# Kernel tuning notes

Hardware: AMD Instinct MI355X
Metric: run time of the kernel (lower is better)

Reference implementation:

```python
import jax, jax.numpy as jnp
import numpy as np

HEADS = 16
LN_EPS = 1e-5

def _ln(v, w, b):
    # LayerNorm over last dim (head dim s)
    mu = jnp.mean(v, axis=-1, keepdims=True)
    var = jnp.mean(jnp.square(v - mu), axis=-1, keepdims=True)
    return (v - mu) * jax.lax.rsqrt(var + LN_EPS) * w + b

def setup_inputs() -> dict:
    key = jax.random.key(0)
    ks = jax.random.split(key, 5)
    b, t, e = 2, 2048, 1024
    x = jax.random.normal(ks[0], (b, t, e), dtype=jnp.float32)
    scale = 0.02
    Wk = jax.random.normal(ks[1], (e, e), dtype=jnp.float32) * scale
    Wq = jax.random.normal(ks[2], (e, e), dtype=jnp.float32) * scale
    Wv = jax.random.normal(ks[3], (e, e), dtype=jnp.float32) * scale
    Wu = jax.random.normal(ks[4], (e, e), dtype=jnp.float32) * scale
    s = e // HEADS
    return {
        "x": x, "Wk": Wk, "Wq": Wq, "Wv": Wv, "Wu": Wu,
        "kln_w": jnp.ones((s,), jnp.float32), "kln_b": jnp.zeros((s,), jnp.float32),
        "qln_w": jnp.ones((s,), jnp.float32), "qln_b": jnp.zeros((s,), jnp.float32),
    }

def reference(x, Wk, Wq, Wv, Wu, kln_w, kln_b, qln_w, qln_b):
    b, t, e = x.shape
    h = HEADS
    s = e // h
    # nn.Linear: y = x @ W^T
    k = (x @ Wk.T).reshape(b, t, h, s)
    q = (x @ Wq.T).reshape(b, t, h, s)
    v = (x @ Wv.T).reshape(b, t, h, s)
    k = _ln(k, kln_w, kln_b)
    q = _ln(q, qln_w, qln_b)
    scalefactor = 1.0 / np.sqrt(s).astype(np.float32)
    # [b, h, t_q, t_k]
    dot = jnp.einsum('bqhs,bkhs->bhqk', q, k) * scalefactor
    causal = jnp.triu(jnp.ones((t, t), dtype=bool), k=1)  # mask strictly-upper (diag kept)
    dot = jnp.where(causal, -jnp.inf, dot)
    attn = jax.nn.softmax(dot, axis=-1)
    out = jnp.einsum('bhqk,bkhs->bqhs', attn, v).reshape(b, t, e)
    return out @ Wu.T
```

## Files before the change

kernel.cpp:

```cpp
#include <hip/hip_runtime.h>
#include <math.h>

#define T_SEQ 2048
#define E_DIM 1024
#define NH    16
#define HS    64
#define NB    2
#define M_ROWS 4096

typedef __attribute__((ext_vector_type(8))) short bf16x8;
typedef __attribute__((ext_vector_type(4))) short bf16x4;
typedef __attribute__((ext_vector_type(4))) float f32x4;

#define AS1 __attribute__((address_space(1)))
#define AS3 __attribute__((address_space(3)))

#define LOG2E 1.4426950408889634f

__device__ __forceinline__ f32x4 mfma16(bf16x4 a, bf16x4 b, f32x4 c) {
    return __builtin_amdgcn_mfma_f32_16x16x16bf16_1k(a, b, c, 0, 0, 0);
}

__device__ __forceinline__ ushort f2bf(float f) {
    union { float f; unsigned u; } c; c.f = f;
    unsigned r = c.u + 0x7fffu + ((c.u >> 16) & 1u);
    return (ushort)(r >> 16);
}
__device__ __forceinline__ ushort f2bf_trunc(float f) {
    union { float f; unsigned u; } c; c.f = f;
    return (ushort)(c.u >> 16);
}

__device__ __forceinline__ void load_lds16(const ushort* g, ushort* l) {
    __builtin_amdgcn_global_load_lds((const AS1 unsigned int*)g,
                                     (AS3 unsigned int*)l, 16, 0, 0);
}

__global__ __launch_bounds__(256) void cvt_all(
    const float* __restrict__ x,  const float* __restrict__ Wk,
    const float* __restrict__ Wq, const float* __restrict__ Wv,
    const float* __restrict__ Wu,
    ushort* __restrict__ xb,  ushort* __restrict__ Wkb,
    ushort* __restrict__ Wqb, ushort* __restrict__ Wvb,
    ushort* __restrict__ Wub)
{
    int i4 = blockIdx.x * 256 + threadIdx.x;
    int region = i4 >> 18;
    const float* src; ushort* dst; int off;
    if      (region < 4)  { src = x;  dst = xb;  off = i4; }
    else if (region == 4) { src = Wk; dst = Wkb; off = i4 - (4 << 18); }
    else if (region == 5) { src = Wq; dst = Wqb; off = i4 - (5 << 18); }
    else if (region == 6) { src = Wv; dst = Wvb; off = i4 - (6 << 18); }
    else                  { src = Wu; dst = Wub; off = i4 - (7 << 18); }
    float4 v = *(const float4*)(src + (size_t)off * 4);
    ushort4 o; o.x = f2bf(v.x); o.y = f2bf(v.y); o.z = f2bf(v.z); o.w = f2bf(v.w);
    *(ushort4*)(dst + (size_t)off * 4) = o;
}

__device__ __forceinline__ void gemm_core_db(
    const ushort* __restrict__ A, const ushort* __restrict__ W,
    int m0, int n0, ushort* As, ushort* Bs, f32x4 acc[4][4])
{
    const int tid  = threadIdx.x;
    const int lane = tid & 63, w = tid >> 6;
    const int quad = lane >> 4, l16 = lane & 15;
    const int wm = w & 1, wn = w >> 1;

    const int rl   = lane >> 2;
    const int gsw  = (lane & 3) ^ ((lane >> 3) & 3);
    const int fsw  = (l16 >> 1) & 3;

    const f32x4 zero = {0.f, 0.f, 0.f, 0.f};
#pragma unroll
    for (int mt = 0; mt < 4; ++mt)
#pragma unroll
        for (int nt = 0; nt < 4; ++nt) acc[mt][nt] = zero;

#pragma unroll
    for (int i = 0; i < 2; ++i) {
        int c = i * 4 + w;
        int row = c * 16 + rl;
        load_lds16(A + (size_t)(m0 + row) * E_DIM + gsw * 8, As + c * 512);
        load_lds16(W + (size_t)(n0 + row) * E_DIM + gsw * 8, Bs + c * 512);
    }

    for (int k0 = 0; k0 < E_DIM; k0 += 32) {
        const int buf = (k0 >> 5) & 1;
        ushort* Ab = As + buf * 4096;
        ushort* Bb = Bs + buf * 4096;
        __syncthreads();
        if (k0 + 32 < E_DIM) {
            ushort* An = As + (buf ^ 1) * 4096;
            ushort* Bn = Bs + (buf ^ 1) * 4096;
#pragma unroll
            for (int i = 0; i < 2; ++i) {
                int c = i * 4 + w;
                int row = c * 16 + rl;
                load_lds16(A + (size_t)(m0 + row) * E_DIM + k0 + 32 + gsw * 8,
                           An + c * 512);
                load_lds16(W + (size_t)(n0 + row) * E_DIM + k0 + 32 + gsw * 8,
                           Bn + c * 512);
            }
        }
        bf16x8 af[4], bfr[4];
#pragma unroll
        for (int mt = 0; mt < 4; ++mt)
            af[mt] = *(const bf16x8*)(Ab + (wm * 64 + mt * 16 + l16) * 32
                                      + ((quad ^ fsw) * 8));
#pragma unroll
        for (int nt = 0; nt < 4; ++nt)
            bfr[nt] = *(const bf16x8*)(Bb + (wn * 64 + nt * 16 + l16) * 32
                                       + ((quad ^ fsw) * 8));
#pragma unroll
        for (int mt = 0; mt < 4; ++mt)
#pragma unroll
            for (int nt = 0; nt < 4; ++nt)
                acc[mt][nt] = __builtin_amdgcn_mfma_f32_16x16x32_bf16(
                    af[mt], bfr[nt], acc[mt][nt], 0, 0, 0);
    }
}

__global__ __launch_bounds__(256) void gemm_qkv(
    const ushort* __restrict__ A,
    const ushort* __restrict__ W0, const ushort* __restrict__ W1,
    const ushort* __restrict__ W2,
    ushort* __restrict__ Kb, ushort* __restrict__ Qb, ushort* __restrict__ Vt,
    const float* __restrict__ kw, const float* __restrict__ kbias,
    const float* __restrict__ qw, const float* __restrict__ qbias)
{
    __shared__ ushort As[2 * 128 * 32];
    __shared__ ushort Bs[2 * 128 * 32];
    const int z = blockIdx.z;
    const ushort* W = (z == 0) ? W0 : (z == 1) ? W1 : W2;
    const int m0 = blockIdx.y * 128, n0 = blockIdx.x * 128;
    f32x4 acc[4][4];
    gemm_core_db(A, W, m0, n0, As, Bs, acc);

    const int lane = threadIdx.x & 63, w = threadIdx.x >> 6;
    const int quad = lane >> 4, l16 = lane & 15;
    const int wm = w & 1, wn = w >> 1;
    const int row0 = m0 + wm * 64;
    const int col0 = n0 + wn * 64;

    if (z < 2) {
        ushort* C = z ? Qb : Kb;
        const float* lw = z ? qw : kw;
        const float* lb = z ? qbias : kbias;
        const float scale = z ? (0.125f * LOG2E) : 1.0f;
        float wv[4], bv_[4];
#pragma unroll
        for (int nt = 0; nt < 4; ++nt) {
            wv[nt]  = lw[nt * 16 + l16];
            bv_[nt] = lb[nt * 16 + l16];
        }
#pragma unroll
        for (int mt = 0; mt < 4; ++mt)
#pragma unroll
            for (int r = 0; r < 4; ++r) {
                float v[4], d[4];
#pragma unroll
                for (int nt = 0; nt < 4; ++nt) v[nt] = acc[mt][nt][r];
                float s = v[0] + v[1] + v[2] + v[3];
                s += __shfl_xor(s, 1); s += __shfl_xor(s, 2);
                s += __shfl_xor(s, 4); s += __shfl_xor(s, 8);
                float mu = s * (1.0f / 64.0f);
                float q2 = 0.f;
#pragma unroll
                for (int nt = 0; nt < 4; ++nt) { d[nt] = v[nt] - mu; q2 += d[nt] * d[nt]; }
                q2 += __shfl_xor(q2, 1); q2 += __shfl_xor(q2, 2);
                q2 += __shfl_xor(q2, 4); q2 += __shfl_xor(q2, 8);
                float rin = rsqrtf(q2 * (1.0f / 64.0f) + 1e-5f);
                int row = row0 + mt * 16 + quad * 4 + r;
#pragma unroll
                for (int nt = 0; nt < 4; ++nt)
                    C[(size_t)row * E_DIM + col0 + nt * 16 + l16] =
                        f2bf((d[nt] * rin * wv[nt] + bv_[nt]) * scale);
            }
    } else {
        const int bidx = m0 >> 11;
        const int hh   = col0 >> 6;
        const int t0   = (m0 & 2047) + wm * 64;
#pragma unroll
        for (int mt = 0; mt < 4; ++mt)
#pragma unroll
            for (int nt = 0; nt < 4; ++nt) {
                ushort4 pk = make_ushort4(f2bf(acc[mt][nt][0]), f2bf(acc[mt][nt][1]),
                                          f2bf(acc[mt][nt][2]), f2bf(acc[mt][nt][3]));
                size_t off = ((size_t)(bidx * NH + hh) * 64 + nt * 16 + l16) * T_SEQ
                             + t0 + mt * 16 + quad * 4;
                *(ushort4*)(Vt + off) = pk;
            }
    }
}

__global__ __launch_bounds__(256) void gemm_o(
    const ushort* __restrict__ A, const ushort* __restrict__ W,
    float* __restrict__ C)
{
    __shared__ ushort As[2 * 128 * 32];
    __shared__ ushort Bs[2 * 128 * 32];
    const int m0 = blockIdx.y * 128, n0 = blockIdx.x * 128;
    f32x4 acc[4][4];
    gemm_core_db(A, W, m0, n0, As, Bs, acc);

    const int lane = threadIdx.x & 63, w = threadIdx.x >> 6;
    const int quad = lane >> 4, l16 = lane & 15;
    const int row0 = m0 + (w & 1) * 64;
    const int col0 = n0 + (w >> 1) * 64;
#pragma unroll
    for (int mt = 0; mt < 4; ++mt)
#pragma unroll
        for (int nt = 0; nt < 4; ++nt)
#pragma unroll
            for (int r = 0; r < 4; ++r)
                C[(size_t)(row0 + mt * 16 + quad * 4 + r) * E_DIM
                  + col0 + nt * 16 + l16] = acc[mt][nt][r];
}

__global__ __launch_bounds__(256, 4) void flash_attn5(
    const ushort* __restrict__ Qg, const ushort* __restrict__ Kg,
    const ushort* __restrict__ Vt, ushort* __restrict__ O)
{
    __shared__ ushort Ks[2][64 * 64];
    __shared__ ushort Vs[2][64 * 64];

    const int tid  = threadIdx.x;
    const int lane = tid & 63, w = tid >> 6;
    const int quad = lane >> 4, l16 = lane & 15;

    const int L = blockIdx.x;
    const int c = L & 255, s = L >> 8;
    const int q0 = c >> 5;
    const int bh = c & 31;
    const int qt = (s == 0) ? q0 : (s == 1) ? (15 - q0)
                 : (s == 2) ? (16 + q0) : (31 - q0);
    const int b = bh >> 4, h = bh & 15;

    const ushort* Qbase = Qg + ((size_t)b * T_SEQ) * E_DIM + h * HS;
    const ushort* Kbase = Kg + ((size_t)b * T_SEQ) * E_DIM + h * HS;
    const ushort* Vbase = Vt + ((size_t)bh * HS) * T_SEQ;

    const int rloc = lane >> 3;
    const int gswc = (lane & 7) ^ rloc;
    const int sw   = l16 & 7;

    bf16x8 aq[2];
#pragma unroll
    for (int ks = 0; ks < 2; ++ks)
        aq[ks] = *(const bf16x8*)(Qbase + (size_t)(qt * 64 + w * 16 + l16) * E_DIM
                                  + ks * 32 + quad * 8);

    const f32x4 zero = {0.f, 0.f, 0.f, 0.f};
    f32x4 o_acc[4];
#pragma unroll
    for (int dt = 0; dt < 4; ++dt) o_acc[dt] = zero;
    float l_acc = 0.f;

#pragma unroll
    for (int i = 0; i < 2; ++i) {
        int cc = w * 2 + i, row = cc * 8 + rloc;
        load_lds16(Kbase + (size_t)row * E_DIM + gswc * 8, Ks[0] + cc * 512);
        load_lds16(Vbase + (size_t)row * T_SEQ + gswc * 8, Vs[0] + cc * 512);
    }

    const float M8 = 8.0f * LOG2E;

    for (int jt = 0; jt <= qt; ++jt) {
        const int buf = jt & 1;
        __syncthreads();
        if (jt < qt) {
#pragma unroll
            for (int i = 0; i < 2; ++i) {
                int cc = w * 2 + i, row = cc * 8 + rloc;
                load_lds16(Kbase + (size_t)(jt + 1) * 64 * E_DIM
                           + (size_t)row * E_DIM + gswc * 8, Ks[buf ^ 1] + cc * 512);
                load_lds16(Vbase + (size_t)row * T_SEQ + (jt + 1) * 64 + gswc * 8,
                           Vs[buf ^ 1] + cc * 512);
            }
        }

        f32x4 sa[4];
#pragma unroll
        for (int nt = 0; nt < 4; ++nt) sa[nt] = zero;
#pragma unroll
        for (int ks = 0; ks < 2; ++ks) {
            int cp = ((ks * 4 + quad) ^ sw) * 8;
#pragma unroll
            for (int nt = 0; nt < 4; ++nt) {
                bf16x8 bk = *(const bf16x8*)(Ks[buf] + (nt * 16 + l16) * 64 + cp);
                sa[nt] = __builtin_amdgcn_mfma_f32_16x16x32_bf16(bk, aq[ks], sa[nt], 0, 0, 0);
            }
        }

        if (jt == qt) {
#pragma unroll
            for (int nt = 0; nt < 4; ++nt)
#pragma unroll
                for (int r = 0; r < 4; ++r)
                    if (nt * 16 + quad * 4 + r > w * 16 + l16) sa[nt][r] = -1e30f;
        }

        bf16x4 bp[4];
#pragma unroll
        for (int nt = 0; nt < 4; ++nt)
#pragma unroll
            for (int r = 0; r < 4; ++r) {
                float p = __builtin_amdgcn_exp2f(sa[nt][r] - M8);
                l_acc += p;
                bp[nt][r] = (short)f2bf_trunc(p);
            }

#pragma unroll
        for (int kt = 0; kt < 4; ++kt) {
            const int tt = kt * 16 + quad * 4;
            const int ch = tt >> 3, el = tt & 7;
#pragma unroll
            for (int dt = 0; dt < 4; ++dt) {
                const int vd = dt * 16 + l16;
                bf16x4 va = *(const bf16x4*)(Vs[buf] + vd * 64
                                             + ((ch ^ (vd & 7)) << 3) + el);
                o_acc[dt] = mfma16(va, bp[kt], o_acc[dt]);
            }
        }
    }

    l_acc += __shfl_xor(l_acc, 16);
    l_acc += __shfl_xor(l_acc, 32);
    const float inv = 1.0f / l_acc;
    const int trow = qt * 64 + w * 16 + l16;
#pragma unroll
    for (int dt = 0; dt < 4; ++dt) {
        ushort4 pk = make_ushort4(f2bf(o_acc[dt][0] * inv), f2bf(o_acc[dt][1] * inv),
                                  f2bf(o_acc[dt][2] * inv), f2bf(o_acc[dt][3] * inv));
        *(ushort4*)(O + ((size_t)b * T_SEQ + trow) * E_DIM + h * HS
                    + dt * 16 + quad * 4) = pk;
    }
}

extern "C" void kernel_launch(void* const* d_in, const int* in_sizes, int n_in,
                              void* d_out, int out_size, void* d_ws, size_t ws_size,
                              hipStream_t stream) {
    const float* x     = (const float*)d_in[0];
    const float* Wk    = (const float*)d_in[1];
    const float* Wq    = (const float*)d_in[2];
    const float* Wv    = (const float*)d_in[3];
    const float* Wu    = (const float*)d_in[4];
    const float* kln_w = (const float*)d_in[5];
    const float* kln_b = (const float*)d_in[6];
    const float* qln_w = (const float*)d_in[7];
    const float* qln_b = (const float*)d_in[8];
    float* out = (float*)d_out;

    const size_t NE = (size_t)M_ROWS * E_DIM;
    const size_t NW = (size_t)E_DIM * E_DIM;
    ushort* xb  = (ushort*)d_ws;
    ushort* Wkb = xb  + NE;
    ushort* Wqb = Wkb + NW;
    ushort* Wvb = Wqb + NW;
    ushort* Wub = Wvb + NW;
    ushort* Kb  = Wub + NW;
    ushort* Qb  = Kb  + NE;
    ushort* Vt  = Qb  + NE;
    ushort* Ob  = Vt  + NE;

    cvt_all<<<8192, 256, 0, stream>>>(x, Wk, Wq, Wv, Wu, xb, Wkb, Wqb, Wvb, Wub);

    gemm_qkv<<<dim3(E_DIM / 128, M_ROWS / 128, 3), 256, 0, stream>>>(
        xb, Wkb, Wqb, Wvb, Kb, Qb, Vt, kln_w, kln_b, qln_w, qln_b);

    flash_attn5<<<1024, 256, 0, stream>>>(Qb, Kb, Vt, Ob);

    gemm_o<<<dim3(E_DIM / 128, M_ROWS / 128), 256, 0, stream>>>(Ob, Wub, out);
}
```

Baseline: 182.0 us.

## Split causal attention KV range across two blocks with a separate merge kernel

Each (batch, head, query tile) is split into two blocks that each process half of the causal KV tiles. The blocks write unnormalized fp32 partial outputs and row sums to a workspace, and a new merge kernel adds the halves, normalizes and writes bf16. Blocks are ordered longest-first and use s_setprio around the MFMA sections, with the row-sum accumulation restructured as a tree. This is meant to balance load and raise parallelism, at the cost of an extra launch plus fp32 partial-result traffic. The shared fixed max offset keeps the merge a simple add.

```diff
diff --git a/kernel.cpp b/kernel.cpp
--- a/kernel.cpp
+++ b/kernel.cpp
@@ -217,9 +217,10 @@
                   + col0 + nt * 16 + l16] = acc[mt][nt][r];
 }
 
-__global__ __launch_bounds__(256, 4) void flash_attn5(
+__global__ __launch_bounds__(256, 4) void flash_attn6(
     const ushort* __restrict__ Qg, const ushort* __restrict__ Kg,
-    const ushort* __restrict__ Vt, ushort* __restrict__ O)
+    const ushort* __restrict__ Vt, float* __restrict__ Pbuf,
+    float* __restrict__ Lbuf)
 {
     __shared__ ushort Ks[2][64 * 64];
     __shared__ ushort Vs[2][64 * 64];
@@ -228,13 +229,19 @@
     const int lane = tid & 63, w = tid >> 6;
     const int quad = lane >> 4, l16 = lane & 15;
 
-    const int L = blockIdx.x;
-    const int c = L & 255, s = L >> 8;
-    const int q0 = c >> 5;
-    const int bh = c & 31;
-    const int qt = (s == 0) ? q0 : (s == 1) ? (15 - q0)
-                 : (s == 2) ? (16 + q0) : (31 - q0);
+    const int pair  = blockIdx.x >> 1;
+    const int split = blockIdx.x & 1;
+    const int bh = pair & 31;
+    const int qt = 31 - (pair >> 5);
     const int b = bh >> 4, h = bh & 15;
+
+    const int ntile = qt + 1;
+    const int hmid  = ntile >> 1;
+    const int jt0 = split ? hmid  : 0;
+    const int jt1 = split ? ntile : hmid;
+    if (jt0 >= jt1) return;
+
+    const int slot = (bh << 5) | qt;
 
     const ushort* Qbase = Qg + ((size_t)b * T_SEQ) * E_DIM + h * HS;
     const ushort* Kbase = Kg + ((size_t)b * T_SEQ) * E_DIM + h * HS;
@@ -259,16 +266,18 @@
 #pragma unroll
     for (int i = 0; i < 2; ++i) {
         int cc = w * 2 + i, row = cc * 8 + rloc;
-        load_lds16(Kbase + (size_t)row * E_DIM + gswc * 8, Ks[0] + cc * 512);
-        load_lds16(Vbase + (size_t)row * T_SEQ + gswc * 8, Vs[0] + cc * 512);
+        load_lds16(Kbase + (size_t)(jt0 * 64 + row) * E_DIM + gswc * 8,
+                   Ks[0] + cc * 512);
+        load_lds16(Vbase + (size_t)row * T_SEQ + jt0 * 64 + gswc * 8,
+                   Vs[0] + cc * 512);
     }
 
     const float M8 = 8.0f * LOG2E;
 
-    for (int jt = 0; jt <= qt; ++jt) {
-        const int buf = jt & 1;
+    for (int jt = jt0; jt < jt1; ++jt) {
+        const int buf = (jt - jt0) & 1;
         __syncthreads();
-        if (jt < qt) {
+        if (jt + 1 < jt1) {
 #pragma unroll
             for (int i = 0; i < 2; ++i) {
                 int cc = w * 2 + i, row = cc * 8 + rloc;
@@ -282,6 +291,7 @@
         f32x4 sa[4];
 #pragma unroll
         for (int nt = 0; nt < 4; ++nt) sa[nt] = zero;
+        __builtin_amdgcn_s_setprio(1);
 #pragma unroll
         for (int ks = 0; ks < 2; ++ks) {
             int cp = ((ks * 4 + quad) ^ sw) * 8;
@@ -291,6 +301,7 @@
                 sa[nt] = __builtin_amdgcn_mfma_f32_16x16x32_bf16(bk, aq[ks], sa[nt], 0, 0, 0);
             }
         }
+        __builtin_amdgcn_s_setprio(0);
 
         if (jt == qt) {
 #pragma unroll
@@ -301,15 +312,22 @@
         }
 
         bf16x4 bp[4];
-#pragma unroll
-        for (int nt = 0; nt < 4; ++nt)
-#pragma unroll
-            for (int r = 0; r < 4; ++r) {
-                float p = __builtin_amdgcn_exp2f(sa[nt][r] - M8);
-                l_acc += p;
-                bp[nt][r] = (short)f2bf_trunc(p);
-            }
-
+        float lp[4];
+#pragma unroll
+        for (int nt = 0; nt < 4; ++nt) {
+            float p0 = __builtin_amdgcn_exp2f(sa[nt][0] - M8);
+            float p1 = __builtin_amdgcn_exp2f(sa[nt][1] - M8);
+            float p2 = __builtin_amdgcn_exp2f(sa[nt][2] - M8);
+            float p3 = __builtin_amdgcn_exp2f(sa[nt][3] - M8);
+            bp[nt][0] = (short)f2bf_trunc(p0);
+            bp[nt][1] = (short)f2bf_trunc(p1);
+            bp[nt][2] = (short)f2bf_trunc(p2);
+            bp[nt][3] = (short)f2bf_trunc(p3);
+            lp[nt] = (p0 + p1) + (p2 + p3);
+        }
+        l_acc += (lp[0] + lp[1]) + (lp[2] + lp[3]);
+
+        __builtin_amdgcn_s_setprio(1);
 #pragma unroll
         for (int kt = 0; kt < 4; ++kt) {
             const int tt = kt * 16 + quad * 4;
@@ -322,18 +340,47 @@
                 o_acc[dt] = mfma16(va, bp[kt], o_acc[dt]);
             }
         }
+        __builtin_amdgcn_s_setprio(0);
     }
 
     l_acc += __shfl_xor(l_acc, 16);
     l_acc += __shfl_xor(l_acc, 32);
-    const float inv = 1.0f / l_acc;
-    const int trow = qt * 64 + w * 16 + l16;
-#pragma unroll
-    for (int dt = 0; dt < 4; ++dt) {
-        ushort4 pk = make_ushort4(f2bf(o_acc[dt][0] * inv), f2bf(o_acc[dt][1] * inv),
-                                  f2bf(o_acc[dt][2] * inv), f2bf(o_acc[dt][3] * inv));
-        *(ushort4*)(O + ((size_t)b * T_SEQ + trow) * E_DIM + h * HS
-                    + dt * 16 + quad * 4) = pk;
+    float* Po = Pbuf + (((size_t)split << 22) | ((size_t)slot << 12));
+    const int q = w * 16 + l16;
+#pragma unroll
+    for (int dt = 0; dt < 4; ++dt)
+        *(f32x4*)(Po + q * 64 + dt * 16 + quad * 4) = o_acc[dt];
+    if (quad == 0) Lbuf[(split << 16) | (slot << 6) | q] = l_acc;
+}
+
+__global__ __launch_bounds__(256) void attn_merge(
+    const float* __restrict__ Pbuf, const float* __restrict__ Lbuf,
+    ushort* __restrict__ O)
+{
+    const int slot = blockIdx.x;
+    const int bh = slot >> 5, qt = slot & 31;
+    const int b = bh >> 4, h = bh & 15;
+    const int tid = threadIdx.x;
+    const int dl = (tid & 15) * 4;
+    const int qh = tid >> 4;
+    const bool has0 = (qt > 0);
+    const float* P0 = Pbuf + ((size_t)slot << 12);
+    const float* P1 = P0 + ((size_t)1 << 22);
+#pragma unroll
+    for (int j = 0; j < 4; ++j) {
+        const int q = j * 16 + qh;
+        float l = Lbuf[(1 << 16) | (slot << 6) | q];
+        if (has0) l += Lbuf[(slot << 6) | q];
+        const float inv = 1.0f / l;
+        float4 c = *(const float4*)(P1 + q * 64 + dl);
+        if (has0) {
+            float4 a = *(const float4*)(P0 + q * 64 + dl);
+            c.x += a.x; c.y += a.y; c.z += a.z; c.w += a.w;
+        }
+        ushort4 pk = make_ushort4(f2bf(c.x * inv), f2bf(c.y * inv),
+                                  f2bf(c.z * inv), f2bf(c.w * inv));
+        *(ushort4*)(O + ((size_t)(b * T_SEQ + qt * 64 + q)) * E_DIM
+                    + h * HS + dl) = pk;
     }
 }
 
@@ -362,13 +409,16 @@
     ushort* Qb  = Kb  + NE;
     ushort* Vt  = Qb  + NE;
     ushort* Ob  = Vt  + NE;
+    float*  Pbuf = (float*)(Ob + NE);
+    float*  Lbuf = Pbuf + ((size_t)2 << 22);
 
     cvt_all<<<8192, 256, 0, stream>>>(x, Wk, Wq, Wv, Wu, xb, Wkb, Wqb, Wvb, Wub);
 
     gemm_qkv<<<dim3(E_DIM / 128, M_ROWS / 128, 3), 256, 0, stream>>>(
         xb, Wkb, Wqb, Wvb, Kb, Qb, Vt, kln_w, kln_b, qln_w, qln_b);
 
-    flash_attn5<<<1024, 256, 0, stream>>>(Qb, Kb, Vt, Ob);
+    flash_attn6<<<2048, 256, 0, stream>>>(Qb, Kb, Vt, Pbuf, Lbuf);
+    attn_merge<<<1024, 256, 0, stream>>>(Pbuf, Lbuf, Ob);
 
     gemm_o<<<dim3(E_DIM / 128, M_ROWS / 128), 256, 0, stream>>>(Ob, Wub, out);
 }
```

Measured after the change: 186.3 us. 1.02x slower.

## Rewrite QKV GEMM as 256x256-tile, 8-wave, 4-stage pipelined kernel

Applied to the files above, without the earlier changes.

Replaces the 128x128 double-buffered QKV GEMM with a 256x256-tile kernel using 512 threads, a 4-deep LDS ring fed by direct global-to-LDS loads, and explicit vmcnt waits and barriers. MFMA phases are interleaved with staging of A and B, with wave priority raised during compute. The three weight matrices are read as one contiguous concatenated Wqkv buffer, and a swizzled block index improves L2 locality. Larger tiles raise arithmetic intensity but need 128 KB of dynamic LDS, which limits occupancy, and the grid shrinks to 192 blocks on a GPU with more CUs than that.

```diff
diff --git a/kernel.cpp b/kernel.cpp
--- a/kernel.cpp
+++ b/kernel.cpp
@@ -120,27 +120,116 @@
     }
 }
 
-__global__ __launch_bounds__(256) void gemm_qkv(
-    const ushort* __restrict__ A,
-    const ushort* __restrict__ W0, const ushort* __restrict__ W1,
-    const ushort* __restrict__ W2,
+__global__ __launch_bounds__(512, 2) void gemm_qkv_8p(
+    const ushort* __restrict__ A, const ushort* __restrict__ Wqkv,
     ushort* __restrict__ Kb, ushort* __restrict__ Qb, ushort* __restrict__ Vt,
     const float* __restrict__ kw, const float* __restrict__ kbias,
     const float* __restrict__ qw, const float* __restrict__ qbias)
 {
-    __shared__ ushort As[2 * 128 * 32];
-    __shared__ ushort Bs[2 * 128 * 32];
-    const int z = blockIdx.z;
-    const ushort* W = (z == 0) ? W0 : (z == 1) ? W1 : W2;
-    const int m0 = blockIdx.y * 128, n0 = blockIdx.x * 128;
-    f32x4 acc[4][4];
-    gemm_core_db(A, W, m0, n0, As, Bs, acc);
-
-    const int lane = threadIdx.x & 63, w = threadIdx.x >> 6;
+    extern __shared__ ushort smem[];
+    ushort* SA = smem;
+    ushort* SB = smem + 4 * 8192;
+
+    const int tid  = threadIdx.x;
+    const int lane = tid & 63, w = tid >> 6;
     const int quad = lane >> 4, l16 = lane & 15;
     const int wm = w & 1, wn = w >> 1;
-    const int row0 = m0 + wm * 64;
-    const int col0 = n0 + wn * 64;
+
+    const int lid = blockIdx.x;
+    const int swz = (lid & 7) * 24 + (lid >> 3);
+    const int m0  = (swz & 15) * 256;
+    const int n0  = (swz >> 4) * 256;
+
+    const int rl  = lane >> 2;
+    const int gsw = (lane & 3) ^ ((lane >> 3) & 3);
+    const int cpq = ((quad ^ ((l16 >> 1) & 3)) * 8);
+
+    const ushort* Ag = A    + (size_t)(m0 + rl) * E_DIM + gsw * 8;
+    const ushort* Bg = Wqkv + (size_t)(n0 + rl) * E_DIM + gsw * 8;
+
+    f32x4 acc[8][4];
+    const f32x4 zero = {0.f, 0.f, 0.f, 0.f};
+#pragma unroll
+    for (int mt = 0; mt < 8; ++mt)
+#pragma unroll
+        for (int nt = 0; nt < 4; ++nt) acc[mt][nt] = zero;
+
+#define STAGE_A8(tt) do {                                                     \
+        const int b_ = (tt) & 3;                                              \
+        _Pragma("unroll")                                                     \
+        for (int i_ = 0; i_ < 2; ++i_) {                                      \
+            const int c_ = i_ * 8 + w;                                        \
+            load_lds16(Ag + (size_t)(c_ * 16) * E_DIM + (tt) * 32,            \
+                       SA + b_ * 8192 + c_ * 512);                            \
+        } } while (0)
+#define STAGE_B8(tt) do {                                                     \
+        const int b_ = (tt) & 3;                                              \
+        _Pragma("unroll")                                                     \
+        for (int i_ = 0; i_ < 2; ++i_) {                                      \
+            const int c_ = i_ * 8 + w;                                        \
+            load_lds16(Bg + (size_t)(c_ * 16) * E_DIM + (tt) * 32,            \
+                       SB + b_ * 8192 + c_ * 512);                            \
+        } } while (0)
+
+#pragma unroll
+    for (int tt = 0; tt < 3; ++tt) { STAGE_A8(tt); STAGE_B8(tt); }
+    asm volatile("s_waitcnt vmcnt(8)" ::: "memory");
+    __builtin_amdgcn_s_barrier();
+    asm volatile("" ::: "memory");
+
+    for (int t = 0; t < 32; ++t) {
+        const ushort* Ab = SA + (t & 3) * 8192;
+        const ushort* Bb = SB + (t & 3) * 8192;
+
+        bf16x8 bfr[4], af[4];
+#pragma unroll
+        for (int nt = 0; nt < 4; ++nt)
+            bfr[nt] = *(const bf16x8*)(Bb + (wn * 64 + nt * 16 + l16) * 32 + cpq);
+#pragma unroll
+        for (int mt = 0; mt < 4; ++mt)
+            af[mt] = *(const bf16x8*)(Ab + (wm * 128 + mt * 16 + l16) * 32 + cpq);
+        if (t + 3 < 32) STAGE_A8(t + 3);
+        __builtin_amdgcn_s_barrier();
+        __builtin_amdgcn_sched_barrier(0);
+        __builtin_amdgcn_s_setprio(1);
+#pragma unroll
+        for (int mt = 0; mt < 4; ++mt)
+#pragma unroll
+            for (int nt = 0; nt < 4; ++nt)
+                acc[mt][nt] = __builtin_amdgcn_mfma_f32_16x16x32_bf16(
+                    af[mt], bfr[nt], acc[mt][nt], 0, 0, 0);
+        __builtin_amdgcn_s_setprio(0);
+        __builtin_amdgcn_s_barrier();
+        asm volatile("" ::: "memory");
+
+        bf16x8 af2[4];
+#pragma unroll
+        for (int mt = 0; mt < 4; ++mt)
+            af2[mt] = *(const bf16x8*)(Ab + (wm * 128 + (4 + mt) * 16 + l16) * 32 + cpq);
+        if (t + 3 < 32) STAGE_B8(t + 3);
+        __builtin_amdgcn_s_barrier();
+        __builtin_amdgcn_sched_barrier(0);
+        __builtin_amdgcn_s_setprio(1);
+#pragma unroll
+        for (int mt = 0; mt < 4; ++mt)
+#pragma unroll
+            for (int nt = 0; nt < 4; ++nt)
+                acc[4 + mt][nt] = __builtin_amdgcn_mfma_f32_16x16x32_bf16(
+                    af2[mt], bfr[nt], acc[4 + mt][nt], 0, 0, 0);
+        __builtin_amdgcn_s_setprio(0);
+        if (t <= 28)      asm volatile("s_waitcnt vmcnt(8)" ::: "memory");
+        else if (t == 29) asm volatile("s_waitcnt vmcnt(4)" ::: "memory");
+        else if (t == 30) asm volatile("s_waitcnt vmcnt(0)" ::: "memory");
+        __builtin_amdgcn_s_barrier();
+        asm volatile("" ::: "memory");
+    }
+#undef STAGE_A8
+#undef STAGE_B8
+
+    const int z    = n0 >> 10;
+    const int ncol = n0 & 1023;
+    const int col0 = ncol + wn * 64;
+    const int row0 = m0 + wm * 128;
 
     if (z < 2) {
         ushort* C = z ? Qb : Kb;
@@ -154,7 +243,7 @@
             bv_[nt] = lb[nt * 16 + l16];
         }
 #pragma unroll
-        for (int mt = 0; mt < 4; ++mt)
+        for (int mt = 0; mt < 8; ++mt)
 #pragma unroll
             for (int r = 0; r < 4; ++r) {
                 float v[4], d[4];
@@ -179,9 +268,9 @@
     } else {
         const int bidx = m0 >> 11;
         const int hh   = col0 >> 6;
-        const int t0   = (m0 & 2047) + wm * 64;
-#pragma unroll
-        for (int mt = 0; mt < 4; ++mt)
+        const int t0   = (m0 & 2047) + wm * 128;
+#pragma unroll
+        for (int mt = 0; mt < 8; ++mt)
 #pragma unroll
             for (int nt = 0; nt < 4; ++nt) {
                 ushort4 pk = make_ushort4(f2bf(acc[mt][nt][0]), f2bf(acc[mt][nt][1]),
@@ -363,10 +452,17 @@
     ushort* Vt  = Qb  + NE;
     ushort* Ob  = Vt  + NE;
 
+    static int attr_done = 0;
+    if (!attr_done) {
+        hipFuncSetAttribute(reinterpret_cast<const void*>(gemm_qkv_8p),
+                            hipFuncAttributeMaxDynamicSharedMemorySize, 131072);
+        attr_done = 1;
+    }
+
     cvt_all<<<8192, 256, 0, stream>>>(x, Wk, Wq, Wv, Wu, xb, Wkb, Wqb, Wvb, Wub);
 
-    gemm_qkv<<<dim3(E_DIM / 128, M_ROWS / 128, 3), 256, 0, stream>>>(
-        xb, Wkb, Wqb, Wvb, Kb, Qb, Vt, kln_w, kln_b, qln_w, qln_b);
+    gemm_qkv_8p<<<192, 512, 131072, stream>>>(
+        xb, Wkb, Kb, Qb, Vt, kln_w, kln_b, qln_w, qln_b);
 
     flash_attn5<<<1024, 256, 0, stream>>>(Qb, Kb, Vt, Ob);
 
```

Result: no change. 185.4 us (+1.9%).
